# Kernel tuning notes

Measured on AMD Instinct MI355X. Metric: run time of the kernel, lower is better.

The kernel has to match this reference:

```python
import jax, jax.numpy as jnp
import numpy as np

jax.config.update("jax_enable_x64", True)

# Module hyperparameters (from init_kwargs)
NUM_EMB = 1_000_000
EMB_DIM = 128
COMPRESSION = 1.0 / 64.0
WEIGHT_SIZE = int(NUM_EMB * EMB_DIM * COMPRESSION)  # 2_000_000 (1D compressed table)

# Hash constants matching the CUDA kernel's multiplicative hash:
# hashed_idx = (index * P1 + dim * P2) mod weight_size
P1 = np.uint64(9824516537)
P2 = np.uint64(57857966300227)

BATCH = 16384
BAG_LEN = 50


def _hashed_idx(indices):
    # indices: [N] int -> hashed positions [N, EMB_DIM] into the 1D weight table
    flat = indices.reshape(-1).astype(jnp.uint64)
    dims = jnp.arange(EMB_DIM, dtype=jnp.uint64)
    h = (flat[:, None] * P1 + dims[None, :] * P2) % jnp.uint64(WEIGHT_SIZE)
    return h.astype(jnp.int64)


def setup_inputs() -> dict:
    key = jax.random.key(0)
    k1, k2 = jax.random.split(key)
    indices = jax.random.randint(k1, (BATCH, BAG_LEN), 0, NUM_EMB, dtype=jnp.int64)
    # reset_parameters(): init.normal_(weight)
    weight = jax.random.normal(k2, (WEIGHT_SIZE,), dtype=jnp.float32)
    return {"weight": weight, "indices": indices}


def reference(weight, indices):
    # 2D indices path: each row is one bag of fixed length; mode='sum'.
    B, L = indices.shape
    hidx = _hashed_idx(indices)                      # [B*L, D]
    emb = weight[hidx].reshape(B, L, EMB_DIM)        # gather from compressed table
    return emb.sum(axis=1)                           # [B, D] per-bag sum
```

## Files before the change

### kernel.cpp

```cpp
#include <hip/hip_runtime.h>
#include <stdint.h>


#define WS       2000000
#define EMB_DIM  128
#define BAG_LEN  50
#define BATCH    16384

#define NBLK     256
#define NTHR     1024
#define BAGS_PB  64
#define NQUAD    16
#define QEXT     408
#define RSZE     65536
#define NREG     31
#define SBIG     300227u
#define SENT     0x10000000u

#define GLOAD_LDS16(gp, lp)                                            \
    __builtin_amdgcn_global_load_lds(                                  \
        (const __attribute__((address_space(1))) uint32_t*)(gp),       \
        (__attribute__((address_space(3))) uint32_t*)(lp), 16, 0, 0)

__global__ __launch_bounds__(1024) void conv_bf16(
    const float* __restrict__ w, uint16_t* __restrict__ o)
{
    const int i = (blockIdx.x * 1024 + threadIdx.x) * 4;
    if (i >= WS) return;
    const float4 f = *(const float4*)(w + i);
    uint32_t u0 = __float_as_uint(f.x), u1 = __float_as_uint(f.y);
    uint32_t u2 = __float_as_uint(f.z), u3 = __float_as_uint(f.w);
    ushort4 r;
    r.x = (uint16_t)((u0 + 0x7FFFu + ((u0 >> 16) & 1u)) >> 16);
    r.y = (uint16_t)((u1 + 0x7FFFu + ((u1 >> 16) & 1u)) >> 16);
    r.z = (uint16_t)((u2 + 0x7FFFu + ((u2 >> 16) & 1u)) >> 16);
    r.w = (uint16_t)((u3 + 0x7FFFu + ((u3 >> 16) & 1u)) >> 16);
    *(ushort4*)(o + i) = r;
}

__global__ __launch_bounds__(NTHR, 4) void heb_bf16(
    const uint16_t* __restrict__ wbf,
    const int*      __restrict__ indices,
    float*          __restrict__ out)
{
    __shared__ __align__(16) uint16_t tile[RSZE];
    __shared__ uint32_t extq[NQUAD][QEXT];

    const int tid     = threadIdx.x;
    const int d       = tid & 127;
    const int g       = tid >> 7;
    const int bagBase = blockIdx.x * BAGS_PB;

    uint32_t* araw = (uint32_t*)&tile[0];
    uint32_t* S    = (uint32_t*)&tile[0] + 4096;

    for (int p = tid; p < NQUAD * QEXT; p += NTHR)
        ((uint32_t*)extq)[p] = SENT;
    for (int p = tid; p < BAGS_PB * BAG_LEN; p += NTHR) {
        uint32_t b = (uint32_t)p / 50u;
        uint32_t i = (uint32_t)p - b * 50u;
        uint64_t idx = (uint64_t)(uint32_t)indices[bagBase * BAG_LEN + p];
        araw[b * 52 + i] = (uint32_t)((idx * 9824516537ull) % (uint64_t)WS);
    }
    __syncthreads();

    for (int p = tid; p < BAGS_PB * BAG_LEN; p += NTHR) {
        uint32_t b = (uint32_t)p / 50u;
        uint32_t i = (uint32_t)p - b * 50u;
        uint32_t v = araw[b * 52 + i];
        int rank = 0;
        for (int q = 0; q < BAG_LEN; ++q) {
            uint32_t w = araw[b * 52 + q];
            rank += (w < v || (w == v && q < (int)i)) ? 1 : 0;
        }
        S[b * 52 + rank] = v;
    }
    __syncthreads();

    for (int p = tid; p < BAGS_PB * BAG_LEN; p += NTHR) {
        uint32_t bag = (uint32_t)p / 50u;
        uint32_t i   = (uint32_t)p - bag * 50u;
        uint32_t qd  = bag >> 2, b = bag & 3u;
        uint32_t v = S[bag * 52 + i];
        int r = (int)i;
        for (uint32_t b2 = 0; b2 < 4u; ++b2) {
            if (b2 == b) continue;
            const uint32_t* T = &S[((qd << 2) + b2) * 52];
            uint32_t key = (b2 < b) ? v + 1u : v;
            int lo = 0, hi = 50;
            while (lo < hi) {
                int mid = (lo + hi) >> 1;
                bool lt = T[mid] < key;
                lo = lt ? mid + 1 : lo;
                hi = lt ? hi : mid;
            }
            r += lo;
        }
        extq[qd][r]       = (v << 2) | b;
        extq[qd][r + 200] = ((v + (uint32_t)WS) << 2) | b;
    }
    __syncthreads();

    const uint32_t c  = ((uint32_t)d * SBIG) % (uint32_t)WS;
    const uint32_t C4 = (uint32_t)(((int)c - WS) * 4);
    const uint32_t limit = ((uint32_t)WS - c) << 2;

    uint32_t t4[2], K[2];
    float sm[2][4];
#pragma unroll
    for (int qi = 0; qi < 2; ++qi) {
        const uint32_t* eg = &extq[(g << 1) + qi][0];
        int lo = 0, hi = 200;
        while (lo < hi) {
            int mid = (lo + hi) >> 1;
            bool lt = eg[mid] < limit;
            lo = lt ? mid + 1 : lo;
            hi = lt ? hi : mid;
        }
        t4[qi] = (uint32_t)lo << 2;
        K[qi]  = eg[lo];
        sm[qi][0] = sm[qi][1] = sm[qi][2] = sm[qi][3] = 0.0f;
    }

    for (int r = 0; r < NREG; ++r) {
        const int lo  = r * RSZE;
        const int len = (RSZE < WS - lo) ? RSZE : (WS - lo);
        __syncthreads();

        for (int s = tid; s < (len >> 3); s += NTHR)
            GLOAD_LDS16(wbf + lo + (s << 3), &tile[s << 3]);
        __syncthreads();

        const uint32_t len4 = (uint32_t)len << 2;
        const uint32_t CL   = C4 - (((uint32_t)lo) << 2);
        const char* tb = (const char*)&tile[0];

#pragma unroll
        for (int qi = 0; qi < 2; ++qi) {
            const char* eg = (const char*)&extq[(g << 1) + qi][0];
            uint32_t t_ = t4[qi], K_ = K[qi];
            uint32_t u  = K_ + CL;
            float s0 = sm[qi][0], s1 = sm[qi][1];
            float s2 = sm[qi][2], s3 = sm[qi][3];
            while (u < len4) {
                const uint32_t raw =
                    *(const uint16_t*)(tb + ((u >> 1) & ~1u));
                const float v = __uint_as_float(raw << 16);
                const uint32_t tag = u & 3u;
                s0 += (tag == 0u) ? v : 0.0f;
                s1 += (tag == 1u) ? v : 0.0f;
                s2 += (tag == 2u) ? v : 0.0f;
                s3 += (tag == 3u) ? v : 0.0f;
                t_ += 4u;
                K_  = *(const uint32_t*)(eg + t_);
                u   = K_ + CL;
            }
            t4[qi] = t_; K[qi] = K_;
            sm[qi][0] = s0; sm[qi][1] = s1; sm[qi][2] = s2; sm[qi][3] = s3;
        }
    }

#pragma unroll
    for (int qi = 0; qi < 2; ++qi)
#pragma unroll
        for (int b = 0; b < 4; ++b) {
            const int bag = (g << 3) + (qi << 2) + b;
            out[(size_t)(bagBase + bag) * EMB_DIM + d] = sm[qi][b];
        }
}

#define RSIZE_FB 32768
#define NREG_FB  62
#define EXT_N    104
#define SENT4    0x10000000u

__global__ __launch_bounds__(NTHR, 4) void heb_single(
    const float* __restrict__ weight,
    const int*   __restrict__ indices,
    float*       __restrict__ out)
{
    __shared__ __align__(16) float tile[RSIZE_FB];
    __shared__ uint32_t ext4[BAGS_PB][EXT_N];
    const int tid = threadIdx.x, d = tid & 127, bag_lo = tid >> 7;
    const int bagBase = blockIdx.x * BAGS_PB;
    uint32_t* araw = (uint32_t*)&tile[0];
    for (int p = tid; p < BAGS_PB * BAG_LEN; p += NTHR) {
        uint32_t g = (uint32_t)p / 50u, i = (uint32_t)p - g * 50u;
        uint64_t idx = (uint64_t)(uint32_t)indices[bagBase * BAG_LEN + p];
        araw[g * 52 + i] = (uint32_t)((idx * 9824516537ull) % (uint64_t)WS);
    }
    __syncthreads();
    for (int p = tid; p < BAGS_PB * BAG_LEN; p += NTHR) {
        uint32_t g = (uint32_t)p / 50u, i = (uint32_t)p - g * 50u;
        uint32_t v = araw[g * 52 + i];
        int rank = 0;
        for (int q = 0; q < BAG_LEN; ++q) {
            uint32_t w = araw[g * 52 + q];
            rank += (w < v || (w == v && q < (int)i)) ? 1 : 0;
        }
        ext4[g][rank] = v << 2;
        ext4[g][rank + 50] = (v + (uint32_t)WS) << 2;
    }
    for (int p = tid; p < BAGS_PB * 4; p += NTHR)
        ext4[p >> 2][100 + (p & 3)] = SENT4;
    __syncthreads();
    const uint32_t c = ((uint32_t)d * SBIG) % (uint32_t)WS;
    const uint32_t C4 = (uint32_t)(((int)c - WS) * 4);
    const uint32_t wmc4 = ((uint32_t)WS - c) << 2;
    uint32_t t4[8], h4[8]; float sm[8];
#pragma unroll
    for (int k = 0; k < 8; ++k) {
        const uint32_t* eg = &ext4[(bag_lo << 3) + k][0];
        int nlow = 0;
        for (int q = 0; q < BAG_LEN; ++q) nlow += (eg[q] < wmc4) ? 1 : 0;
        t4[k] = (uint32_t)nlow << 2; h4[k] = eg[nlow] + C4; sm[k] = 0.0f;
    }
    for (int r = 0; r < NREG_FB; ++r) {
        const int lo = r * RSIZE_FB;
        const int len = (RSIZE_FB < WS - lo) ? RSIZE_FB : (WS - lo);
        __syncthreads();
        for (int s = tid; s < (len >> 2); s += NTHR)
            GLOAD_LDS16(weight + lo + (s << 2), &tile[s << 2]);
        __syncthreads();
        const uint32_t lo4 = ((uint32_t)lo) << 2;
        const uint32_t hi4 = (r == NREG_FB - 1) ? (uint32_t)(4 * WS)
                                                : lo4 + ((uint32_t)RSIZE_FB << 2);
        const char* tb = (const char*)&tile[0];
#pragma unroll
        for (int k = 0; k < 8; ++k) {
            const char* eg = (const char*)&ext4[(bag_lo << 3) + k][0];
            uint32_t t_ = t4[k], h_ = h4[k]; float s_ = sm[k];
            while (h_ < hi4) {
                s_ += *(const float*)(tb + (h_ - lo4));
                t_ += 4u;
                h_ = *(const uint32_t*)(eg + t_) + C4;
            }
            t4[k] = t_; h4[k] = h_; sm[k] = s_;
        }
    }
#pragma unroll
    for (int k = 0; k < 8; ++k)
        out[(size_t)(bagBase + (bag_lo << 3) + k) * EMB_DIM + d] = sm[k];
}

extern "C" void kernel_launch(void* const* d_in, const int* in_sizes, int n_in,
                              void* d_out, int out_size, void* d_ws, size_t ws_size,
                              hipStream_t stream)
{
    const float* weight  = (const float*)d_in[0];
    const int*   indices = (const int*)d_in[1];
    float*       out     = (float*)d_out;

    if (ws_size >= (size_t)WS * sizeof(uint16_t)) {
        uint16_t* wbf = (uint16_t*)d_ws;
        conv_bf16<<<(WS / 4 + 1023) / 1024, 1024, 0, stream>>>(weight, wbf);
        heb_bf16<<<NBLK, NTHR, 0, stream>>>(wbf, indices, out);
    } else {
        heb_single<<<NBLK, NTHR, 0, stream>>>(weight, indices, out);
    }
}
```

Measured before the change: 228.3 us.

## Double-buffer bf16 table regions and merge bags into octets with LDS atomic accumulation

```diff
diff --git a/kernel.cpp b/kernel.cpp
--- a/kernel.cpp
+++ b/kernel.cpp
@@ -10,12 +10,17 @@
 #define NBLK     256
 #define NTHR     1024
 #define BAGS_PB  64
-#define NQUAD    16
-#define QEXT     408
-#define RSZE     65536
-#define NREG     31
+#define NOCT     8
+#define EXT8     808
+#define THALF    24576
+#define NREGD    82
 #define SBIG     300227u
 #define SENT     0x10000000u
+
+#define OFF_T1   49152
+#define OFF_ACC  98304
+#define OFF_EXT  131072
+#define SMEM_SZ  156928
 
 #define GLOAD_LDS16(gp, lp)                                            \
     __builtin_amdgcn_global_load_lds(                                  \
@@ -43,19 +48,24 @@
     const int*      __restrict__ indices,
     float*          __restrict__ out)
 {
-    __shared__ __align__(16) uint16_t tile[RSZE];
-    __shared__ uint32_t extq[NQUAD][QEXT];
+    __shared__ __align__(16) uint8_t smem[SMEM_SZ];
 
     const int tid     = threadIdx.x;
     const int d       = tid & 127;
     const int g       = tid >> 7;
     const int bagBase = blockIdx.x * BAGS_PB;
 
-    uint32_t* araw = (uint32_t*)&tile[0];
-    uint32_t* S    = (uint32_t*)&tile[0] + 4096;
-
-    for (int p = tid; p < NQUAD * QEXT; p += NTHR)
-        ((uint32_t*)extq)[p] = SENT;
+    uint16_t* tile0 = (uint16_t*)&smem[0];
+    float*    acc   = (float*)&smem[OFF_ACC];
+    uint32_t* ext   = (uint32_t*)&smem[OFF_EXT];
+    uint32_t* araw  = (uint32_t*)&smem[OFF_T1];
+    uint32_t* S     = (uint32_t*)&smem[OFF_T1 + 16384];
+
+    for (int s = tid; s < (THALF >> 3); s += NTHR)
+        GLOAD_LDS16(wbf + (s << 3), tile0 + (s << 3));
+
+    for (int p = tid; p < NOCT * EXT8; p += NTHR) ext[p] = SENT;
+    for (int p = tid; p < BAGS_PB * EMB_DIM; p += NTHR) acc[p] = 0.0f;
     for (int p = tid; p < BAGS_PB * BAG_LEN; p += NTHR) {
         uint32_t b = (uint32_t)p / 50u;
         uint32_t i = (uint32_t)p - b * 50u;
@@ -80,12 +90,12 @@
     for (int p = tid; p < BAGS_PB * BAG_LEN; p += NTHR) {
         uint32_t bag = (uint32_t)p / 50u;
         uint32_t i   = (uint32_t)p - bag * 50u;
-        uint32_t qd  = bag >> 2, b = bag & 3u;
+        uint32_t oct = bag >> 3, b = bag & 7u;
         uint32_t v = S[bag * 52 + i];
-        int r = (int)i;
-        for (uint32_t b2 = 0; b2 < 4u; ++b2) {
+        int rk = (int)i;
+        for (uint32_t b2 = 0; b2 < 8u; ++b2) {
             if (b2 == b) continue;
-            const uint32_t* T = &S[((qd << 2) + b2) * 52];
+            const uint32_t* T = &S[((oct << 3) + b2) * 52];
             uint32_t key = (b2 < b) ? v + 1u : v;
             int lo = 0, hi = 50;
             while (lo < hi) {
@@ -94,79 +104,63 @@
                 lo = lt ? mid + 1 : lo;
                 hi = lt ? hi : mid;
             }
-            r += lo;
-        }
-        extq[qd][r]       = (v << 2) | b;
-        extq[qd][r + 200] = ((v + (uint32_t)WS) << 2) | b;
+            rk += lo;
+        }
+        uint32_t* eo = ext + oct * EXT8;
+        eo[rk]       = (v << 3) | b;
+        eo[rk + 400] = ((v + (uint32_t)WS) << 3) | b;
     }
     __syncthreads();
 
     const uint32_t c  = ((uint32_t)d * SBIG) % (uint32_t)WS;
-    const uint32_t C4 = (uint32_t)(((int)c - WS) * 4);
-    const uint32_t limit = ((uint32_t)WS - c) << 2;
-
-    uint32_t t4[2], K[2];
-    float sm[2][4];
-#pragma unroll
-    for (int qi = 0; qi < 2; ++qi) {
-        const uint32_t* eg = &extq[(g << 1) + qi][0];
-        int lo = 0, hi = 200;
-        while (lo < hi) {
-            int mid = (lo + hi) >> 1;
-            bool lt = eg[mid] < limit;
-            lo = lt ? mid + 1 : lo;
-            hi = lt ? hi : mid;
-        }
-        t4[qi] = (uint32_t)lo << 2;
-        K[qi]  = eg[lo];
-        sm[qi][0] = sm[qi][1] = sm[qi][2] = sm[qi][3] = 0.0f;
-    }
-
-    for (int r = 0; r < NREG; ++r) {
-        const int lo  = r * RSZE;
-        const int len = (RSZE < WS - lo) ? RSZE : (WS - lo);
+    const uint32_t C8 = (uint32_t)(((int)c - WS) * 8);
+    const uint32_t limit = ((uint32_t)WS - c) << 3;
+    const uint32_t* eo = ext + g * EXT8;
+    int lo = 0, hi = 400;
+    while (lo < hi) {
+        int mid = (lo + hi) >> 1;
+        bool lt = eo[mid] < limit;
+        lo = lt ? mid + 1 : lo;
+        hi = lt ? hi : mid;
+    }
+    const char* kp = (const char*)(eo + lo);
+    uint32_t K = *(const uint32_t*)kp;
+    float* accT = acc + (g << 10) + d;
+    __syncthreads();
+
+    for (int r = 0; r < NREGD; ++r) {
+        if (r + 1 < NREGD) {
+            const int lo2  = (r + 1) * THALF;
+            const int len2 = (THALF < WS - lo2) ? THALF : (WS - lo2);
+            uint16_t* dst = (uint16_t*)&smem[((r + 1) & 1) ? OFF_T1 : 0];
+            for (int s = tid; s < (len2 >> 3); s += NTHR)
+                GLOAD_LDS16(wbf + lo2 + (s << 3), dst + (s << 3));
+        }
+
+        const int rlo = r * THALF;
+        const int len = (THALF < WS - rlo) ? THALF : (WS - rlo);
+        const uint32_t TB4 = (r & 1) ? ((uint32_t)OFF_T1 << 2) : 0u;
+        const uint32_t CLr = C8 + TB4 - ((uint32_t)rlo << 3);
+        const uint32_t LIM = ((uint32_t)len << 3) + TB4;
+
+        uint32_t u = K + CLr;
+        while (u < LIM) {
+            const uint32_t baddr = (u >> 2) & ~1u;
+            kp += 4;
+            const uint32_t Kn = *(const uint32_t*)kp;
+            const uint32_t raw = *(const uint16_t*)(smem + baddr);
+            atomicAdd(accT + ((u & 7u) << 7),
+                      __uint_as_float(raw << 16));
+            K = Kn;
+            u = Kn + CLr;
+        }
         __syncthreads();
-
-        for (int s = tid; s < (len >> 3); s += NTHR)
-            GLOAD_LDS16(wbf + lo + (s << 3), &tile[s << 3]);
-        __syncthreads();
-
-        const uint32_t len4 = (uint32_t)len << 2;
-        const uint32_t CL   = C4 - (((uint32_t)lo) << 2);
-        const char* tb = (const char*)&tile[0];
-
-#pragma unroll
-        for (int qi = 0; qi < 2; ++qi) {
-            const char* eg = (const char*)&extq[(g << 1) + qi][0];
-            uint32_t t_ = t4[qi], K_ = K[qi];
-            uint32_t u  = K_ + CL;
-            float s0 = sm[qi][0], s1 = sm[qi][1];
-            float s2 = sm[qi][2], s3 = sm[qi][3];
-            while (u < len4) {
-                const uint32_t raw =
-                    *(const uint16_t*)(tb + ((u >> 1) & ~1u));
-                const float v = __uint_as_float(raw << 16);
-                const uint32_t tag = u & 3u;
-                s0 += (tag == 0u) ? v : 0.0f;
-                s1 += (tag == 1u) ? v : 0.0f;
-                s2 += (tag == 2u) ? v : 0.0f;
-                s3 += (tag == 3u) ? v : 0.0f;
-                t_ += 4u;
-                K_  = *(const uint32_t*)(eg + t_);
-                u   = K_ + CL;
-            }
-            t4[qi] = t_; K[qi] = K_;
-            sm[qi][0] = s0; sm[qi][1] = s1; sm[qi][2] = s2; sm[qi][3] = s3;
-        }
-    }
-
-#pragma unroll
-    for (int qi = 0; qi < 2; ++qi)
-#pragma unroll
-        for (int b = 0; b < 4; ++b) {
-            const int bag = (g << 3) + (qi << 2) + b;
-            out[(size_t)(bagBase + bag) * EMB_DIM + d] = sm[qi][b];
-        }
+    }
+
+#pragma unroll
+    for (int b = 0; b < 8; ++b)
+        out[(size_t)(bagBase + (g << 3) + b) * EMB_DIM + d] =
+            acc[((g << 3) + b) * EMB_DIM + d];
 }
 
 #define RSIZE_FB 32768
```

Measured after the change: 715.1 us. 3.13x slower.
